# Performance work log

Measured on AMD Instinct MI355X. Metric: run time of the kernel, lower is better.

Reference implementation:

```python
import jax, jax.numpy as jnp
import numpy as np

B = 4096      # batch of states
N = 32        # SVGD particles per state
D_ACT = 16    # action dim
D_OBS = 64    # obs dim
H = 256       # critic hidden width
STEPS = 3     # num_svgd_steps
LR = 0.1      # svgd_lr
LIMIT = 1.0   # act_limit


def q_mlp(obs, x, w1, b1, w2, b2, w3, b3):
    # SAC-style critic: q(obs, a) -> scalar per row. obs/x: [BN, *]
    h = jnp.concatenate([obs, x], axis=-1)
    h = jax.nn.relu(h @ w1 + b1)
    h = jax.nn.relu(h @ w2 + b2)
    return (h @ w3 + b3)[..., 0]  # [BN]


def rbf_kernel(X, Y):
    # X: [B, N, D] (differentiable), Y: [B, N, D] (detached copy of X)
    diff = X[:, :, None, :] - Y[:, None, :, :]          # [B, N, N, D]
    dist_sq = jnp.sum(diff * diff, axis=-1)             # [B, N, N]
    # median heuristic bandwidth per batch element
    med = jnp.median(dist_sq.reshape(dist_sq.shape[0], -1), axis=-1)
    h = med / np.log(N) + 1e-8
    gamma = jax.lax.stop_gradient(1.0 / (2.0 * h))      # [B]
    K = jnp.exp(-gamma[:, None, None] * dist_sq)        # [B, N, N]
    # dK/dX (grad wrt first argument)
    K_grad = -2.0 * gamma[:, None, None, None] * diff * K[..., None]  # [B,N,N,D]
    return K, diff, gamma, K_grad


def setup_inputs() -> dict:
    key = jax.random.key(0)
    ks = jax.random.split(key, 6)
    BN = B * N
    sc = lambda k, shp: jax.random.normal(k, shp, jnp.float32) * 0.05
    return {
        "obs": jax.random.normal(ks[0], (BN, D_OBS), jnp.float32),
        "a": jax.random.normal(ks[1], (BN, D_ACT), jnp.float32),
        "w1": sc(ks[2], (D_OBS + D_ACT, H)),
        "b1": jnp.zeros((H,), jnp.float32),
        "w2": sc(ks[3], (H, H)),
        "b2": jnp.zeros((H,), jnp.float32),
        "w3": sc(ks[4], (H, 1)),
        "b3": jnp.zeros((1,), jnp.float32),
    }


def reference(obs, a, w1, b1, w2, b2, w3, b3):
    # a0 arrives detached in the original (sampler(obs, a0.detach(), ...))
    a = jax.lax.stop_gradient(a)
    logp = jnp.zeros((B, N), jnp.float32)
    q_fn = lambda X: q_mlp(obs, X, w1, b1, w2, b2, w3, b3)
    q_vals = None
    for _ in range(STEPS):
        # log_prob = min(q1, q1) == q1; score = d(sum q)/dX via vjp
        q_vals, vjp_fn = jax.vjp(q_fn, a)                 # q_vals: [BN]
        score, = vjp_fn(jnp.ones_like(q_vals))            # [BN, D_ACT]
        X = a.reshape(B, N, D_ACT)
        S = score.reshape(B, N, D_ACT)
        K, diff, gamma, K_grad = rbf_kernel(X, jax.lax.stop_gradient(X))
        # phi = (K.detach() @ score - K_grad.sum(2)) / N
        drive = jnp.einsum('bij,bjd->bid', jax.lax.stop_gradient(K), S)
        phi = (drive - K_grad.sum(axis=2)) / N            # [B, N, D]
        # logp correction terms
        tmp1 = (K_grad * S[:, None, :, :]).sum(-1).mean(-1)                 # [B, N]
        tmp2 = -2.0 * gamma[:, None] * (((-K_grad) * diff).sum(-1)
                                        - D_ACT * K).mean(-1)               # [B, N]
        logp = logp - LR * (tmp1 + tmp2)
        # svgd_optim + clamp + detach
        a = a + LR * phi.reshape(B * N, D_ACT)
        a = jax.lax.stop_gradient(jnp.clip(a, -LIMIT, LIMIT))
    return a.reshape(B, N, D_ACT), logp, q_vals
```

## Files before the change

### kernel.cpp

```cpp
#include <hip/hip_runtime.h>
#include <hip/hip_bf16.h>
#include <math.h>

#define BNROWS (4096*32)
#define RB     64
#define LN32   3.4657359027997265f

typedef __attribute__((ext_vector_type(8))) short bf16x8;
typedef __attribute__((ext_vector_type(4))) float f32x4;

static __device__ __forceinline__ ushort f2bf(float x) {
    union { __hip_bfloat16 h; ushort u; } cv;
    cv.h = __float2bfloat16(x);
    return cv.u;
}

__global__ void prep_pack(const float* __restrict__ w1,
                          const float* __restrict__ w2,
                          ushort* __restrict__ pB1, ushort* __restrict__ pB2,
                          ushort* __restrict__ pB3, ushort* __restrict__ pB4) {
    int g = blockIdx.x * 256 + threadIdx.x;
    ushort out[8];
    ushort* dst;
    if (g < 3072) {
        int lane = g & 63, gc = g >> 6;
        int t = gc / 3, c = gc % 3;
        int m = lane & 15, q = lane >> 4, n = t * 16 + m;
        #pragma unroll
        for (int j = 0; j < 8; ++j) {
            int k = c * 32 + q * 8 + j;
            out[j] = f2bf((k < 80) ? w1[k * 256 + n] : 0.f);
        }
        dst = &pB1[g * 8];
    } else if (g < 11264) {
        int gg = g - 3072;
        int lane = gg & 63, gc = gg >> 6;
        int t = gc >> 3, c = gc & 7;
        int m = lane & 15, q = lane >> 4, n = t * 16 + m;
        #pragma unroll
        for (int j = 0; j < 8; ++j)
            out[j] = f2bf(w2[(c * 32 + q * 8 + j) * 256 + n]);
        dst = &pB2[gg * 8];
    } else if (g < 19456) {
        int gg = g - 11264;
        int lane = gg & 63, gc = gg >> 6;
        int t = gc >> 3, c = gc & 7;
        int m = lane & 15, q = lane >> 4;
        #pragma unroll
        for (int j = 0; j < 8; ++j)
            out[j] = f2bf(w2[(t * 16 + m) * 256 + c * 32 + q * 8 + j]);
        dst = &pB3[gg * 8];
    } else if (g < 19968) {
        int gg = g - 19456;
        int lane = gg & 63, c = gg >> 6;
        int m = lane & 15, q = lane >> 4;
        #pragma unroll
        for (int j = 0; j < 8; ++j)
            out[j] = f2bf(w1[(64 + m) * 256 + c * 32 + q * 8 + j]);
        dst = &pB4[gg * 8];
    } else return;
    *(uint4*)dst = *(uint4*)out;
}

__global__ __launch_bounds__(512) void mlp_mfma(
    const float* __restrict__ obs,
    const float* __restrict__ a_in,
    const float* __restrict__ b1,
    const float* __restrict__ b2,
    const float* __restrict__ w3,
    const float* __restrict__ b3,
    const ushort* __restrict__ pB1, const ushort* __restrict__ pB2,
    const ushort* __restrict__ pB3, const ushort* __restrict__ pB4,
    float* __restrict__ score,
    float* __restrict__ qout,
    int wantq)
{
    __shared__ __align__(16) ushort B0[RB * 264];
    __shared__ __align__(16) ushort B1s[RB * 104];
    __shared__ float qpart[8][RB];
    __shared__ float bias1[256], bias2[256], w3s[256];

    const int tid  = threadIdx.x;
    const int row0 = blockIdx.x * RB;

    {
        int r = tid >> 3, ch = tid & 7;
        const float* op = &obs[(size_t)(row0 + r) * 64 + ch * 8];
        float4 v0 = *(const float4*)op;
        float4 v1 = *(const float4*)(op + 4);
        ushort o[8];
        o[0] = f2bf(v0.x); o[1] = f2bf(v0.y); o[2] = f2bf(v0.z); o[3] = f2bf(v0.w);
        o[4] = f2bf(v1.x); o[5] = f2bf(v1.y); o[6] = f2bf(v1.z); o[7] = f2bf(v1.w);
        *(uint4*)&B1s[r * 104 + ch * 8] = *(uint4*)o;
    }
    if (tid < 256) {
        int r = tid >> 2, d0 = (tid & 3) * 4;
        float4 av = *(const float4*)&a_in[(size_t)(row0 + r) * 16 + d0];
        ushort4 pv;
        pv.x = f2bf(av.x); pv.y = f2bf(av.y); pv.z = f2bf(av.z); pv.w = f2bf(av.w);
        *(ushort4*)&B1s[r * 104 + 64 + d0] = pv;
        ushort4 zv; zv.x = zv.y = zv.z = zv.w = 0;
        *(ushort4*)&B1s[r * 104 + 80 + d0] = zv;
        bias1[tid] = b1[tid]; bias2[tid] = b2[tid]; w3s[tid] = w3[tid];
    }
    __syncthreads();

    const int lane = tid & 63;
    const int w    = tid >> 6;
    const int m    = lane & 15;
    const int q    = lane >> 4;
    const int qk   = q * 8;

    f32x4 acc[4][2];
    unsigned relumask = 0u;

    #pragma unroll
    for (int tc = 0; tc < 2; ++tc)
        #pragma unroll
        for (int rt = 0; rt < 4; ++rt) acc[rt][tc] = (f32x4){0.f, 0.f, 0.f, 0.f};
    for (int c = 0; c < 3; ++c) {
        bf16x8 af[4];
        #pragma unroll
        for (int rt = 0; rt < 4; ++rt)
            af[rt] = *(const bf16x8*)&B1s[(rt * 16 + m) * 104 + c * 32 + qk];
        #pragma unroll
        for (int tc = 0; tc < 2; ++tc) {
            bf16x8 wfr = *(const bf16x8*)&pB1[(((w * 2 + tc) * 3 + c) * 64 + lane) * 8];
            #pragma unroll
            for (int rt = 0; rt < 4; ++rt)
                acc[rt][tc] = __builtin_amdgcn_mfma_f32_16x16x32_bf16(wfr, af[rt], acc[rt][tc], 0, 0, 0);
        }
    }
    #pragma unroll
    for (int tc = 0; tc < 2; ++tc) {
        const float4 bv = *(const float4*)&bias1[(w * 2 + tc) * 16 + q * 4];
        const float bva[4] = {bv.x, bv.y, bv.z, bv.w};
        #pragma unroll
        for (int rt = 0; rt < 4; ++rt) {
            ushort4 pk;
            float z0 = acc[rt][tc][0] + bva[0];
            float z1 = acc[rt][tc][1] + bva[1];
            float z2 = acc[rt][tc][2] + bva[2];
            float z3 = acc[rt][tc][3] + bva[3];
            if (z0 > 0.f) relumask |= 1u << (rt * 8 + tc * 4 + 0);
            if (z1 > 0.f) relumask |= 1u << (rt * 8 + tc * 4 + 1);
            if (z2 > 0.f) relumask |= 1u << (rt * 8 + tc * 4 + 2);
            if (z3 > 0.f) relumask |= 1u << (rt * 8 + tc * 4 + 3);
            pk.x = f2bf(fmaxf(z0, 0.f)); pk.y = f2bf(fmaxf(z1, 0.f));
            pk.z = f2bf(fmaxf(z2, 0.f)); pk.w = f2bf(fmaxf(z3, 0.f));
            *(ushort4*)&B0[(rt * 16 + m) * 264 + (w * 2 + tc) * 16 + q * 4] = pk;
        }
    }
    __syncthreads();

    #pragma unroll
    for (int tc = 0; tc < 2; ++tc)
        #pragma unroll
        for (int rt = 0; rt < 4; ++rt) acc[rt][tc] = (f32x4){0.f, 0.f, 0.f, 0.f};
    for (int c = 0; c < 8; ++c) {
        bf16x8 af[4];
        #pragma unroll
        for (int rt = 0; rt < 4; ++rt)
            af[rt] = *(const bf16x8*)&B0[(rt * 16 + m) * 264 + c * 32 + qk];
        #pragma unroll
        for (int tc = 0; tc < 2; ++tc) {
            bf16x8 wfr = *(const bf16x8*)&pB2[(((w * 2 + tc) * 8 + c) * 64 + lane) * 8];
            #pragma unroll
            for (int rt = 0; rt < 4; ++rt)
                acc[rt][tc] = __builtin_amdgcn_mfma_f32_16x16x32_bf16(wfr, af[rt], acc[rt][tc], 0, 0, 0);
        }
    }
    __syncthreads();
    {
        float qp[4] = {0.f, 0.f, 0.f, 0.f};
        #pragma unroll
        for (int tc = 0; tc < 2; ++tc) {
            const float4 bv = *(const float4*)&bias2[(w * 2 + tc) * 16 + q * 4];
            const float4 wv = *(const float4*)&w3s[(w * 2 + tc) * 16 + q * 4];
            const float bva[4] = {bv.x, bv.y, bv.z, bv.w};
            const float wva[4] = {wv.x, wv.y, wv.z, wv.w};
            #pragma unroll
            for (int rt = 0; rt < 4; ++rt) {
                ushort4 pk; float dz[4];
                #pragma unroll
                for (int i = 0; i < 4; ++i) {
                    float z = acc[rt][tc][i] + bva[i];
                    if (z > 0.f) { qp[rt] += z * wva[i]; dz[i] = wva[i]; }
                    else         { dz[i] = 0.f; }
                }
                pk.x = f2bf(dz[0]); pk.y = f2bf(dz[1]);
                pk.z = f2bf(dz[2]); pk.w = f2bf(dz[3]);
                *(ushort4*)&B0[(rt * 16 + m) * 264 + (w * 2 + tc) * 16 + q * 4] = pk;
            }
        }
        if (wantq) {
            #pragma unroll
            for (int rt = 0; rt < 4; ++rt) {
                float v = qp[rt];
                v += __shfl_xor(v, 16); v += __shfl_xor(v, 32);
                if (q == 0) qpart[w][rt * 16 + m] = v;
            }
        }
    }
    __syncthreads();

    if (wantq && tid < RB) {
        float qs = b3[0];
        #pragma unroll
        for (int ww = 0; ww < 8; ++ww) qs += qpart[ww][tid];
        qout[row0 + tid] = qs;
    }

    #pragma unroll
    for (int tc = 0; tc < 2; ++tc)
        #pragma unroll
        for (int rt = 0; rt < 4; ++rt) acc[rt][tc] = (f32x4){0.f, 0.f, 0.f, 0.f};
    for (int c = 0; c < 8; ++c) {
        bf16x8 af[4];
        #pragma unroll
        for (int rt = 0; rt < 4; ++rt)
            af[rt] = *(const bf16x8*)&B0[(rt * 16 + m) * 264 + c * 32 + qk];
        #pragma unroll
        for (int tc = 0; tc < 2; ++tc) {
            bf16x8 wfr = *(const bf16x8*)&pB3[(((w * 2 + tc) * 8 + c) * 64 + lane) * 8];
            #pragma unroll
            for (int rt = 0; rt < 4; ++rt)
                acc[rt][tc] = __builtin_amdgcn_mfma_f32_16x16x32_bf16(wfr, af[rt], acc[rt][tc], 0, 0, 0);
        }
    }
    __syncthreads();
    #pragma unroll
    for (int rt = 0; rt < 4; ++rt)
        #pragma unroll
        for (int tc = 0; tc < 2; ++tc) {
            ushort4 pk;
            pk.x = f2bf((relumask >> (rt * 8 + tc * 4 + 0)) & 1u ? acc[rt][tc][0] : 0.f);
            pk.y = f2bf((relumask >> (rt * 8 + tc * 4 + 1)) & 1u ? acc[rt][tc][1] : 0.f);
            pk.z = f2bf((relumask >> (rt * 8 + tc * 4 + 2)) & 1u ? acc[rt][tc][2] : 0.f);
            pk.w = f2bf((relumask >> (rt * 8 + tc * 4 + 3)) & 1u ? acc[rt][tc][3] : 0.f);
            *(ushort4*)&B0[(rt * 16 + m) * 264 + (w * 2 + tc) * 16 + q * 4] = pk;
        }
    __syncthreads();

    if (w < 4) {
        f32x4 acc2 = (f32x4){0.f, 0.f, 0.f, 0.f};
        for (int c = 0; c < 8; ++c) {
            bf16x8 af = *(const bf16x8*)&B0[(w * 16 + m) * 264 + c * 32 + qk];
            bf16x8 wfr = *(const bf16x8*)&pB4[(c * 64 + lane) * 8];
            acc2 = __builtin_amdgcn_mfma_f32_16x16x32_bf16(wfr, af, acc2, 0, 0, 0);
        }
        float4 o; o.x = acc2[0]; o.y = acc2[1]; o.z = acc2[2]; o.w = acc2[3];
        *(float4*)&score[(size_t)(row0 + w * 16 + m) * 16 + q * 4] = o;
    }
}

__global__ __launch_bounds__(256, 2) void svgd6(
    const float* __restrict__ a_in,
    const float* __restrict__ score,
    const float* __restrict__ logp_in,
    float* __restrict__ logp_out,
    float* __restrict__ a_out,
    int first)
{
    __shared__ __align__(16) float X4[4][32 * 20];
    __shared__ __align__(16) float S4[4][32 * 20];
    __shared__ __align__(16) float KM4[4][1024];

    const int tid    = threadIdx.x;
    const int wv     = tid >> 6;
    const int lane   = tid & 63;
    const int stateg = blockIdx.x * 4 + wv;
    const size_t base = (size_t)stateg * 512;

    float* X  = X4[wv];
    float* S  = S4[wv];
    float* KM = KM4[wv];

    {
        int g0 = lane * 8;
        int r = g0 >> 4, d0 = g0 & 15;
        float4 va0 = *(const float4*)&a_in[base + g0];
        float4 va1 = *(const float4*)&a_in[base + g0 + 4];
        float4 vs0 = *(const float4*)&score[base + g0];
        float4 vs1 = *(const float4*)&score[base + g0 + 4];
        *(float4*)&X[r * 20 + d0]     = va0;
        *(float4*)&X[r * 20 + d0 + 4] = va1;
        *(float4*)&S[r * 20 + d0]     = vs0;
        *(float4*)&S[r * 20 + d0 + 4] = vs1;
    }
    __asm__ volatile("s_waitcnt lgkmcnt(0)" ::: "memory");

    const int half = lane >> 5;
    const int j    = lane & 31;

    float Xj[16], Sj[16];
    #pragma unroll
    for (int d0 = 0; d0 < 16; d0 += 4) {
        float4 xv = *(const float4*)&X[j * 20 + d0];
        float4 sv = *(const float4*)&S[j * 20 + d0];
        Xj[d0 + 0] = xv.x; Xj[d0 + 1] = xv.y; Xj[d0 + 2] = xv.z; Xj[d0 + 3] = xv.w;
        Sj[d0 + 0] = sv.x; Sj[d0 + 1] = sv.y; Sj[d0 + 2] = sv.z; Sj[d0 + 3] = sv.w;
    }

    unsigned v[16]; float p[16];
    #pragma unroll 4
    for (int t = 0; t < 16; ++t) {
        const float* Xi = &X[(half * 16 + t) * 20];
        float ss = 0.f, pp = 0.f;
        #pragma unroll
        for (int d0 = 0; d0 < 16; d0 += 4) {
            float4 xv = *(const float4*)&Xi[d0];
            float df0 = xv.x - Xj[d0 + 0];
            float df1 = xv.y - Xj[d0 + 1];
            float df2 = xv.z - Xj[d0 + 2];
            float df3 = xv.w - Xj[d0 + 3];
            ss = fmaf(df0, df0, ss); pp = fmaf(df0, Sj[d0 + 0], pp);
            ss = fmaf(df1, df1, ss); pp = fmaf(df1, Sj[d0 + 1], pp);
            ss = fmaf(df2, df2, ss); pp = fmaf(df2, Sj[d0 + 2], pp);
            ss = fmaf(df3, df3, ss); pp = fmaf(df3, Sj[d0 + 3], pp);
        }
        v[t] = __float_as_uint(ss);
        p[t] = pp;
    }

    unsigned vmin, vmax;
    {
        unsigned mn = 0xFFFFFFFFu, mx = 0u;
        #pragma unroll
        for (int t = 0; t < 16; ++t) {
            mn = min(mn, v[t]); mx = max(mx, v[t]);
        }
        #pragma unroll
        for (int off = 1; off < 64; off <<= 1) {
            mn = min(mn, (unsigned)__shfl_xor((int)mn, off));
            mx = max(mx, (unsigned)__shfl_xor((int)mx, off));
        }
        vmin = mn; vmax = mx;
    }
    unsigned lo = vmin, hi = vmax;
    while (lo < hi) {
        unsigned mid = lo + ((hi - lo) >> 1);
        int c = 0;
        #pragma unroll
        for (int t = 0; t < 16; ++t) c += (v[t] <= mid) ? 1 : 0;
        #pragma unroll
        for (int off = 1; off < 64; off <<= 1) c += __shfl_xor(c, off);
        if (c >= 512) hi = mid; else lo = mid + 1;
    }
    const unsigned prefix = lo;
    const float v1 = __uint_as_float(prefix);

    int cle = 0;
    unsigned mgt = 0xFFFFFFFFu;
    #pragma unroll
    for (int t = 0; t < 16; ++t) {
        if (v[t] <= prefix) cle++;
        else mgt = min(mgt, v[t]);
    }
    #pragma unroll
    for (int off = 1; off < 64; off <<= 1) {
        cle += __shfl_xor(cle, off);
        mgt = min(mgt, (unsigned)__shfl_xor((int)mgt, off));
    }
    const float v2  = (cle >= 513) ? v1 : __uint_as_float(mgt);
    const float med = 0.5f * (v1 + v2);
    const float gamma = 1.0f / (2.0f * (med / LN32 + 1e-8f));

    #pragma unroll 4
    for (int t = 0; t < 16; ++t) {
        int i = half * 16 + t;
        float kk = __expf(-gamma * __uint_as_float(v[t]));
        KM[i * 32 + (j ^ i)] = kk;
        float acc = fmaf(fmaf(2.f * gamma, __uint_as_float(v[t]), -16.f), kk,
                         kk * p[t]);
        #pragma unroll
        for (int off = 1; off < 32; off <<= 1)
            acc += __shfl_xor(acc, off);
        if (j == 0) {
            float tmp = -2.f * gamma * acc * (1.f / 32.f);
            float prev = first ? 0.f : logp_in[stateg * 32 + i];
            logp_out[stateg * 32 + i] = prev - 0.1f * tmp;
        }
    }
    __asm__ volatile("s_waitcnt lgkmcnt(0)" ::: "memory");

    {
        const int d  = lane & 15;
        const int i0 = lane >> 4;
        float s1[8], s2[8], xi[8];
        #pragma unroll
        for (int e = 0; e < 8; ++e) {
            s1[e] = 0.f; s2[e] = 0.f;
            xi[e] = X[(i0 + 4 * e) * 20 + d];
        }
        for (int jj = 0; jj < 32; ++jj) {
            float xjv = X[jj * 20 + d];
            float sjv = S[jj * 20 + d];
            #pragma unroll
            for (int e = 0; e < 8; ++e) {
                int i = i0 + 4 * e;
                float kk = KM[i * 32 + (jj ^ i)];
                s1[e] = fmaf(kk, sjv, s1[e]);
                s2[e] = fmaf(kk, xi[e] - xjv, s2[e]);
            }
        }
        #pragma unroll
        for (int e = 0; e < 8; ++e) {
            int i = i0 + 4 * e;
            float phi = (s1[e] + 2.f * gamma * s2[e]) * (1.f / 32.f);
            float av = xi[e] + 0.1f * phi;
            av = fminf(fmaxf(av, -1.f), 1.f);
            a_out[base + i * 16 + d] = av;
        }
    }
}

extern "C" void kernel_launch(void* const* d_in, const int* in_sizes, int n_in,
                              void* d_out, int out_size, void* d_ws, size_t ws_size,
                              hipStream_t stream) {
    const float* obs = (const float*)d_in[0];
    const float* a0  = (const float*)d_in[1];
    const float* w1  = (const float*)d_in[2];
    const float* b1  = (const float*)d_in[3];
    const float* w2  = (const float*)d_in[4];
    const float* b2  = (const float*)d_in[5];
    const float* w3  = (const float*)d_in[6];
    const float* b3  = (const float*)d_in[7];

    float* out_a    = (float*)d_out;
    float* out_logp = out_a + (size_t)BNROWS * 16;
    float* out_q    = out_logp + BNROWS;

    char* p = (char*)d_ws;
    ushort* pB1 = (ushort*)p; p += 24576 * 2;
    ushort* pB2 = (ushort*)p; p += 65536 * 2;
    ushort* pB3 = (ushort*)p; p += 65536 * 2;
    ushort* pB4 = (ushort*)p; p += 4096 * 2;
    float* abuf0 = (float*)p; p += (size_t)BNROWS * 16 * 4;
    float* abuf1 = (float*)p; p += (size_t)BNROWS * 16 * 4;
    float* scr   = (float*)p; p += (size_t)BNROWS * 16 * 4;
    float* logp  = (float*)p; p += (size_t)BNROWS * 4;
    float* qtmp  = (float*)p;

    prep_pack<<<78, 256, 0, stream>>>(w1, w2, pB1, pB2, pB3, pB4);

    const int MB = BNROWS / RB;
    const int SB = 4096 / 4;

    mlp_mfma<<<MB, 512, 0, stream>>>(obs, a0, b1, b2, w3, b3,
                                     pB1, pB2, pB3, pB4, scr, qtmp, 0);
    svgd6<<<SB, 256, 0, stream>>>(a0, scr, nullptr, logp, abuf0, 1);
    mlp_mfma<<<MB, 512, 0, stream>>>(obs, abuf0, b1, b2, w3, b3,
                                     pB1, pB2, pB3, pB4, scr, qtmp, 0);
    svgd6<<<SB, 256, 0, stream>>>(abuf0, scr, logp, logp, abuf1, 0);
    mlp_mfma<<<MB, 512, 0, stream>>>(obs, abuf1, b1, b2, w3, b3,
                                     pB1, pB2, pB3, pB4, scr, out_q, 1);
    svgd6<<<SB, 256, 0, stream>>>(abuf1, scr, logp, out_logp, out_a, 0);
}
```

Measured before the change: 322.5 us.

## Fuse SVGD update into critic MLP kernel, keeping score in LDS

Merges the SVGD update kernel into the MLP kernel. Each 64-row block now covers two states, and the score goes to shared memory (reusing the MLP buffers) instead of a global scratch buffer. This removes three kernel launches and the global round trip of the score array. The trade-off is that only 2 of the 8 waves do the SVGD phase while the rest exit. The pairwise distance loop is also reordered to walk dimensions in the outer loop with per-pair accumulators.

New measurement: 474.9 us. 1.47x slower.

```diff
diff --git a/kernel.cpp b/kernel.cpp
--- a/kernel.cpp
+++ b/kernel.cpp
@@ -62,7 +62,7 @@
     *(uint4*)dst = *(uint4*)out;
 }
 
-__global__ __launch_bounds__(512) void mlp_mfma(
+__global__ __launch_bounds__(512) void fused_step(
     const float* __restrict__ obs,
     const float* __restrict__ a_in,
     const float* __restrict__ b1,
@@ -71,14 +71,19 @@
     const float* __restrict__ b3,
     const ushort* __restrict__ pB1, const ushort* __restrict__ pB2,
     const ushort* __restrict__ pB3, const ushort* __restrict__ pB4,
-    float* __restrict__ score,
+    const float* __restrict__ logp_in,
+    float* __restrict__ logp_out,
+    float* __restrict__ a_out,
     float* __restrict__ qout,
-    int wantq)
+    int first, int wantq)
 {
     __shared__ __align__(16) ushort B0[RB * 264];
     __shared__ __align__(16) ushort B1s[RB * 104];
     __shared__ float qpart[8][RB];
     __shared__ float bias1[256], bias2[256], w3s[256];
+
+    float* OV = (float*)B1s;
+    float* KMOV = (float*)B0;
 
     const int tid  = threadIdx.x;
     const int row0 = blockIdx.x * RB;
@@ -249,80 +254,58 @@
             bf16x8 wfr = *(const bf16x8*)&pB4[(c * 64 + lane) * 8];
             acc2 = __builtin_amdgcn_mfma_f32_16x16x32_bf16(wfr, af, acc2, 0, 0, 0);
         }
+        int row = w * 16 + m;
+        int st  = row >> 5, sr = row & 31;
         float4 o; o.x = acc2[0]; o.y = acc2[1]; o.z = acc2[2]; o.w = acc2[3];
-        *(float4*)&score[(size_t)(row0 + w * 16 + m) * 16 + q * 4] = o;
-    }
-}
-
-__global__ __launch_bounds__(256, 2) void svgd6(
-    const float* __restrict__ a_in,
-    const float* __restrict__ score,
-    const float* __restrict__ logp_in,
-    float* __restrict__ logp_out,
-    float* __restrict__ a_out,
-    int first)
-{
-    __shared__ __align__(16) float X4[4][32 * 20];
-    __shared__ __align__(16) float S4[4][32 * 20];
-    __shared__ __align__(16) float KM4[4][1024];
-
-    const int tid    = threadIdx.x;
-    const int wv     = tid >> 6;
-    const int lane   = tid & 63;
-    const int stateg = blockIdx.x * 4 + wv;
+        *(float4*)&OV[1280 + st * 640 + sr * 20 + q * 4] = o;
+    }
+    __syncthreads();
+
+    if (w >= 2) return;
+
+    const int stateg  = blockIdx.x * 2 + w;
     const size_t base = (size_t)stateg * 512;
-
-    float* X  = X4[wv];
-    float* S  = S4[wv];
-    float* KM = KM4[wv];
+    float* X  = OV + w * 640;
+    float* S  = OV + 1280 + w * 640;
+    float* KM = KMOV + w * 1024;
 
     {
         int g0 = lane * 8;
         int r = g0 >> 4, d0 = g0 & 15;
         float4 va0 = *(const float4*)&a_in[base + g0];
         float4 va1 = *(const float4*)&a_in[base + g0 + 4];
-        float4 vs0 = *(const float4*)&score[base + g0];
-        float4 vs1 = *(const float4*)&score[base + g0 + 4];
         *(float4*)&X[r * 20 + d0]     = va0;
         *(float4*)&X[r * 20 + d0 + 4] = va1;
-        *(float4*)&S[r * 20 + d0]     = vs0;
-        *(float4*)&S[r * 20 + d0 + 4] = vs1;
     }
     __asm__ volatile("s_waitcnt lgkmcnt(0)" ::: "memory");
 
     const int half = lane >> 5;
     const int j    = lane & 31;
 
-    float Xj[16], Sj[16];
-    #pragma unroll
+    float ss[16], pp[16];
+    #pragma unroll
+    for (int t = 0; t < 16; ++t) { ss[t] = 0.f; pp[t] = 0.f; }
+    #pragma unroll 1
     for (int d0 = 0; d0 < 16; d0 += 4) {
-        float4 xv = *(const float4*)&X[j * 20 + d0];
-        float4 sv = *(const float4*)&S[j * 20 + d0];
-        Xj[d0 + 0] = xv.x; Xj[d0 + 1] = xv.y; Xj[d0 + 2] = xv.z; Xj[d0 + 3] = xv.w;
-        Sj[d0 + 0] = sv.x; Sj[d0 + 1] = sv.y; Sj[d0 + 2] = sv.z; Sj[d0 + 3] = sv.w;
-    }
-
-    unsigned v[16]; float p[16];
-    #pragma unroll 4
-    for (int t = 0; t < 16; ++t) {
-        const float* Xi = &X[(half * 16 + t) * 20];
-        float ss = 0.f, pp = 0.f;
-        #pragma unroll
-        for (int d0 = 0; d0 < 16; d0 += 4) {
-            float4 xv = *(const float4*)&Xi[d0];
-            float df0 = xv.x - Xj[d0 + 0];
-            float df1 = xv.y - Xj[d0 + 1];
-            float df2 = xv.z - Xj[d0 + 2];
-            float df3 = xv.w - Xj[d0 + 3];
-            ss = fmaf(df0, df0, ss); pp = fmaf(df0, Sj[d0 + 0], pp);
-            ss = fmaf(df1, df1, ss); pp = fmaf(df1, Sj[d0 + 1], pp);
-            ss = fmaf(df2, df2, ss); pp = fmaf(df2, Sj[d0 + 2], pp);
-            ss = fmaf(df3, df3, ss); pp = fmaf(df3, Sj[d0 + 3], pp);
-        }
-        v[t] = __float_as_uint(ss);
-        p[t] = pp;
-    }
-
+        float4 xj = *(const float4*)&X[j * 20 + d0];
+        float4 sj = *(const float4*)&S[j * 20 + d0];
+        #pragma unroll
+        for (int t = 0; t < 16; ++t) {
+            float4 xi = *(const float4*)&X[(half * 16 + t) * 20 + d0];
+            float df0 = xi.x - xj.x, df1 = xi.y - xj.y;
+            float df2 = xi.z - xj.z, df3 = xi.w - xj.w;
+            ss[t] = fmaf(df0, df0, ss[t]); pp[t] = fmaf(df0, sj.x, pp[t]);
+            ss[t] = fmaf(df1, df1, ss[t]); pp[t] = fmaf(df1, sj.y, pp[t]);
+            ss[t] = fmaf(df2, df2, ss[t]); pp[t] = fmaf(df2, sj.z, pp[t]);
+            ss[t] = fmaf(df3, df3, ss[t]); pp[t] = fmaf(df3, sj.w, pp[t]);
+        }
+    }
+    unsigned v[16];
+    #pragma unroll
+    for (int t = 0; t < 16; ++t) v[t] = __float_as_uint(ss[t]);
+
+    {
+    }
     unsigned vmin, vmax;
     {
         unsigned mn = 0xFFFFFFFFu, mx = 0u;
@@ -371,13 +354,13 @@
         int i = half * 16 + t;
         float kk = __expf(-gamma * __uint_as_float(v[t]));
         KM[i * 32 + (j ^ i)] = kk;
-        float acc = fmaf(fmaf(2.f * gamma, __uint_as_float(v[t]), -16.f), kk,
-                         kk * p[t]);
+        float acc2 = fmaf(fmaf(2.f * gamma, __uint_as_float(v[t]), -16.f), kk,
+                          kk * pp[t]);
         #pragma unroll
         for (int off = 1; off < 32; off <<= 1)
-            acc += __shfl_xor(acc, off);
+            acc2 += __shfl_xor(acc2, off);
         if (j == 0) {
-            float tmp = -2.f * gamma * acc * (1.f / 32.f);
+            float tmp = -2.f * gamma * acc2 * (1.f / 32.f);
             float prev = first ? 0.f : logp_in[stateg * 32 + i];
             logp_out[stateg * 32 + i] = prev - 0.1f * tmp;
         }
@@ -438,22 +421,20 @@
     ushort* pB4 = (ushort*)p; p += 4096 * 2;
     float* abuf0 = (float*)p; p += (size_t)BNROWS * 16 * 4;
     float* abuf1 = (float*)p; p += (size_t)BNROWS * 16 * 4;
-    float* scr   = (float*)p; p += (size_t)BNROWS * 16 * 4;
     float* logp  = (float*)p; p += (size_t)BNROWS * 4;
     float* qtmp  = (float*)p;
 
     prep_pack<<<78, 256, 0, stream>>>(w1, w2, pB1, pB2, pB3, pB4);
 
     const int MB = BNROWS / RB;
-    const int SB = 4096 / 4;
-
-    mlp_mfma<<<MB, 512, 0, stream>>>(obs, a0, b1, b2, w3, b3,
-                                     pB1, pB2, pB3, pB4, scr, qtmp, 0);
-    svgd6<<<SB, 256, 0, stream>>>(a0, scr, nullptr, logp, abuf0, 1);
-    mlp_mfma<<<MB, 512, 0, stream>>>(obs, abuf0, b1, b2, w3, b3,
-                                     pB1, pB2, pB3, pB4, scr, qtmp, 0);
-    svgd6<<<SB, 256, 0, stream>>>(abuf0, scr, logp, logp, abuf1, 0);
-    mlp_mfma<<<MB, 512, 0, stream>>>(obs, abuf1, b1, b2, w3, b3,
-                                     pB1, pB2, pB3, pB4, scr, out_q, 1);
-    svgd6<<<SB, 256, 0, stream>>>(abuf1, scr, logp, out_logp, out_a, 0);
+
+    fused_step<<<MB, 512, 0, stream>>>(obs, a0, b1, b2, w3, b3,
+                                       pB1, pB2, pB3, pB4,
+                                       nullptr, logp, abuf0, qtmp, 1, 0);
+    fused_step<<<MB, 512, 0, stream>>>(obs, abuf0, b1, b2, w3, b3,
+                                       pB1, pB2, pB3, pB4,
+                                       logp, logp, abuf1, qtmp, 0, 0);
+    fused_step<<<MB, 512, 0, stream>>>(obs, abuf1, b1, b2, w3, b3,
+                                       pB1, pB2, pB3, pB4,
+                                       logp, out_logp, out_a, out_q, 0, 1);
 }
```
